# Kernel optimization log

Hardware: AMD Instinct MI355X
Metric: run time of the kernel (lower is better)

## Reference

```python
import math
import jax, jax.numpy as jnp
import numpy as np

B, T, D, H, HD, FF = 2, 2048, 768, 12, 64, 3072


def setup_inputs() -> dict:
    key = jax.random.key(0)
    ks = jax.random.split(key, 9)
    s = 0.02  # init scale
    x = jax.random.normal(ks[0], (B, T, D), jnp.float32)
    wq = jax.random.normal(ks[1], (D, D), jnp.float32) * s
    wk = jax.random.normal(ks[2], (D, D), jnp.float32) * s
    wv = jax.random.normal(ks[3], (D, D), jnp.float32) * s
    wo = jax.random.normal(ks[4], (D, D), jnp.float32) * s
    w1 = jax.random.normal(ks[5], (FF, D), jnp.float32) * s
    w2 = jax.random.normal(ks[6], (FF, D), jnp.float32) * s
    w3 = jax.random.normal(ks[7], (D, FF), jnp.float32) * s
    attn_norm_w = jnp.ones((D,), jnp.float32)
    ffn_norm_w = jnp.ones((D,), jnp.float32)
    # interleaved RoPE cache: values pair-repeated along head_dim
    inv_freq = 1.0 / (10000.0 ** (np.arange(0, HD, 2, dtype=np.float32) / HD))
    freqs = np.arange(T, dtype=np.float32)[:, None] * inv_freq[None, :]  # [T, HD/2]
    emb = np.repeat(freqs, 2, axis=-1)  # [T, HD]
    cos = jnp.asarray(np.cos(emb), jnp.float32)[None, None]  # [1,1,T,HD]
    sin = jnp.asarray(np.sin(emb), jnp.float32)[None, None]
    return {"x": x, "wq": wq, "wk": wk, "wv": wv, "wo": wo,
            "w1": w1, "w2": w2, "w3": w3,
            "attn_norm_w": attn_norm_w, "ffn_norm_w": ffn_norm_w,
            "cos": cos, "sin": sin}


def _rmsnorm(x, w, eps=1e-6):
    n = jnp.linalg.norm(x, axis=-1, keepdims=True)
    return w * x / (n / math.sqrt(x.shape[-1]) + eps)


def _rotate_half(x):
    x1, x2 = x[..., ::2], x[..., 1::2]
    return jnp.stack((-x2, x1), axis=-1).reshape(x.shape)


def _attention(x, wq, wk, wv, wo, cos, sin):
    b, t, c = x.shape
    q = (x @ wq.T).reshape(b, t, H, HD).transpose(0, 2, 1, 3)  # [B,H,T,hd]
    k = (x @ wk.T).reshape(b, t, H, HD).transpose(0, 2, 1, 3)
    v = (x @ wv.T).reshape(b, t, H, HD).transpose(0, 2, 1, 3)
    c_, s_ = cos[:, :, :t, :], sin[:, :, :t, :]
    q = q * c_ + _rotate_half(q) * s_
    k = k * c_ + _rotate_half(k) * s_
    att = jnp.einsum('bhqd,bhkd->bhqk', q, k) / math.sqrt(HD)
    mask = jnp.triu(jnp.full((t, t), -jnp.inf, att.dtype), k=1)
    att = jax.nn.softmax(att + mask, axis=-1)
    y = jnp.einsum('bhqk,bhkd->bhqd', att, v)
    y = y.transpose(0, 2, 1, 3).reshape(b, t, c)
    return y @ wo.T


def reference(x, wq, wk, wv, wo, w1, w2, w3, attn_norm_w, ffn_norm_w, cos, sin):
    x = x + _attention(_rmsnorm(x, attn_norm_w), wq, wk, wv, wo, cos, sin)
    h = _rmsnorm(x, ffn_norm_w)
    ff = (jax.nn.silu(h @ w1.T) * (h @ w2.T)) @ w3.T
    return x + ff
```

## Files before the change

kernel.cpp:

```cpp
#include <hip/hip_runtime.h>
#include <hip/hip_bf16.h>
#include <math.h>

typedef __bf16 bf16;
typedef __bf16 bf16x4 __attribute__((ext_vector_type(4)));
typedef __bf16 bf16x8 __attribute__((ext_vector_type(8)));
typedef float floatx4 __attribute__((ext_vector_type(4)));

#define T_ 2048
#define D_ 768
#define H_ 12
#define HD_ 64
#define FF_ 3072
#define LOG2E 1.44269504f
#define LDP 72

__device__ __forceinline__ floatx4 mfma_bf16(bf16x8 a, bf16x8 b, floatx4 c) {
  return __builtin_amdgcn_mfma_f32_16x16x32_bf16(a, b, c, 0, 0, 0);
}

__device__ __forceinline__ void rms_row(const float* __restrict__ x,
                                        const float* __restrict__ wt,
                                        bf16* __restrict__ o, int row, int tid) {
  const long off = (long)row * D_;
  float vals[3];
  float ss = 0.f;
#pragma unroll
  for (int i = 0; i < 3; i++) {
    vals[i] = x[off + tid + i * 256];
    ss += vals[i] * vals[i];
  }
#pragma unroll
  for (int d = 1; d < 64; d <<= 1) ss += __shfl_xor(ss, d);
  __shared__ float wsum[4];
  if ((tid & 63) == 0) wsum[tid >> 6] = ss;
  __syncthreads();
  const float tot = wsum[0] + wsum[1] + wsum[2] + wsum[3];
  const float inv = 1.0f / (sqrtf(tot * (1.0f / 768.0f)) + 1e-6f);
#pragma unroll
  for (int i = 0; i < 3; i++)
    o[off + tid + i * 256] = (bf16)(vals[i] * inv * wt[tid + i * 256]);
}

__global__ __launch_bounds__(256)
void prep_k(const float* __restrict__ wq, const float* __restrict__ wk,
            const float* __restrict__ wv, const float* __restrict__ wo,
            const float* __restrict__ w1, const float* __restrict__ w2,
            const float* __restrict__ w3, bf16* __restrict__ o,
            const float* __restrict__ x, const float* __restrict__ anw,
            bf16* __restrict__ hn) {
  if (blockIdx.x >= 4608) {
    rms_row(x, anw, hn, blockIdx.x - 4608, threadIdx.x);
    return;
  }
  const long i = ((long)blockIdx.x * 256 + threadIdx.x) * 8;
  const float* s;
  if      (i <  589824) s = wq + i;
  else if (i < 1179648) s = wk + (i -  589824);
  else if (i < 1769472) s = wv + (i - 1179648);
  else if (i < 2359296) s = wo + (i - 1769472);
  else if (i < 4718592) s = w1 + (i - 2359296);
  else if (i < 7077888) s = w2 + (i - 4718592);
  else                  s = w3 + (i - 7077888);
  const floatx4 a = *(const floatx4*)s;
  const floatx4 b = *(const floatx4*)(s + 4);
  bf16x8 r;
#pragma unroll
  for (int j = 0; j < 4; j++) { r[j] = (bf16)a[j]; r[4 + j] = (bf16)b[j]; }
  *(bf16x8*)&o[i] = r;
}

__global__ __launch_bounds__(256)
void rmsnorm_k(const float* __restrict__ x, const float* __restrict__ wt,
               bf16* __restrict__ o) {
  rms_row(x, wt, o, blockIdx.x, threadIdx.x);
}

__global__ __launch_bounds__(256)
void gemm_qkv(const bf16* __restrict__ A, const bf16* __restrict__ wq,
              const bf16* __restrict__ wk, const bf16* __restrict__ wv,
              bf16* __restrict__ q, bf16* __restrict__ k, bf16* __restrict__ vt,
              const float* __restrict__ cosb, const float* __restrict__ sinb) {
  const int widx = blockIdx.x / 6;
  const int nb   = blockIdx.x % 6;
  const bf16* W = (widx == 0) ? wq : (widx == 1) ? wk : wv;
  const int m0 = blockIdx.y * 128, n0 = nb * 128;
  const int K = D_;

  __shared__ __align__(16) bf16 As[128 * LDP];
  __shared__ __align__(16) bf16 Ws[128 * LDP];

  const int tid = threadIdx.x;
  const int lane = tid & 63;
  const int wm = tid >> 7;
  const int wn = (tid >> 6) & 1;
  const int fr = lane & 15;
  const int fk = (lane >> 4) * 8;

  floatx4 acc[4][4] = {};

  const int ar = tid >> 3;
  const int ac = (tid & 7) * 8;
  const bf16* Aptr = A + (long)(m0 + ar) * K + ac;
  const bf16* Wptr = W + (long)(n0 + ar) * K + ac;
  const long rstep = (long)32 * K;

  bf16x8 apf[4], wpf[4];
#pragma unroll
  for (int c = 0; c < 4; c++) apf[c] = *(const bf16x8*)(Aptr + c * rstep);
#pragma unroll
  for (int c = 0; c < 4; c++) wpf[c] = *(const bf16x8*)(Wptr + c * rstep);

  const int ns = K >> 6;
  for (int ks = 0; ks < ns; ks++) {
    __syncthreads();
#pragma unroll
    for (int c = 0; c < 4; c++) *(bf16x8*)&As[(ar + c * 32) * LDP + ac] = apf[c];
#pragma unroll
    for (int c = 0; c < 4; c++) *(bf16x8*)&Ws[(ar + c * 32) * LDP + ac] = wpf[c];
    __syncthreads();
    const long koff = (long)((ks + 1 < ns) ? ks + 1 : ks) * 64;
#pragma unroll
    for (int c = 0; c < 4; c++) apf[c] = *(const bf16x8*)(Aptr + koff + c * rstep);
#pragma unroll
    for (int c = 0; c < 4; c++) wpf[c] = *(const bf16x8*)(Wptr + koff + c * rstep);
#pragma unroll
    for (int kc = 0; kc < 2; kc++) {
      bf16x8 af[4], bfv[4];
#pragma unroll
      for (int i = 0; i < 4; i++) af[i]  = *(const bf16x8*)&As[(wm * 64 + i * 16 + fr) * LDP + kc * 32 + fk];
#pragma unroll
      for (int j = 0; j < 4; j++) bfv[j] = *(const bf16x8*)&Ws[(wn * 64 + j * 16 + fr) * LDP + kc * 32 + fk];
#pragma unroll
      for (int i = 0; i < 4; i++)
#pragma unroll
        for (int j = 0; j < 4; j++)
          acc[i][j] = mfma_bf16(af[i], bfv[j], acc[i][j]);
    }
  }

  const int rb = (lane >> 4) * 4;
  if (widx < 2) {
    bf16* O = (widx == 0) ? q : k;
    const float sgn = (fr & 1) ? 1.f : -1.f;
#pragma unroll
    for (int i = 0; i < 4; i++)
#pragma unroll
      for (int j = 0; j < 4; j++) {
        const int n = n0 + wn * 64 + j * 16 + fr;
        const int d = n & 63;
#pragma unroll
        for (int r = 0; r < 4; r++) {
          const int m = m0 + wm * 64 + i * 16 + rb + r;
          const int pos = m & (T_ - 1);
          const float val = acc[i][j][r];
          const float par = __shfl_xor(val, 1);
          const float cc = cosb[pos * HD_ + d];
          const float ss = sinb[pos * HD_ + d];
          O[(long)m * D_ + n] = (bf16)(val * cc + sgn * par * ss);
        }
      }
  } else {
#pragma unroll
    for (int i = 0; i < 4; i++)
#pragma unroll
      for (int j = 0; j < 4; j++) {
        const int n = n0 + wn * 64 + j * 16 + fr;
        const int m = m0 + wm * 64 + i * 16 + rb;
        const int b = m >> 11;
        const int t = m & (T_ - 1);
        const long row = (long)(b * H_ + (n >> 6)) * HD_ + (n & 63);
        bf16x4 pk;
#pragma unroll
        for (int r = 0; r < 4; r++) pk[r] = (bf16)acc[i][j][r];
        *(bf16x4*)&vt[row * T_ + t] = pk;
      }
  }
}

__global__ __launch_bounds__(256)
void gemm_n64(const bf16* __restrict__ A, const bf16* __restrict__ W,
              float* __restrict__ C, const float* __restrict__ resid,
              int N, int K) {
  __shared__ __align__(16) bf16 As[128 * LDP];
  __shared__ __align__(16) bf16 Ws[64 * LDP];

  const int L  = blockIdx.x;
  const int j  = L >> 3;
  const int mb = (L & 7) * 4 + (j / 12);
  const int nb = j % 12;
  const int m0 = mb * 128, n0 = nb * 64;

  const int tid = threadIdx.x;
  const int lane = tid & 63;
  const int wm = tid >> 7;
  const int wn = (tid >> 6) & 1;
  const int fr = lane & 15;
  const int fk = (lane >> 4) * 8;

  floatx4 acc[4][2] = {};

  const int ar = tid >> 3;
  const int ac = (tid & 7) * 8;
  const bf16* Aptr = A + (long)(m0 + ar) * K + ac;
  const bf16* Wptr = W + (long)(n0 + ar) * K + ac;
  const long rstep = (long)32 * K;

  bf16x8 apf[4], wpf[2];
#pragma unroll
  for (int c = 0; c < 4; c++) apf[c] = *(const bf16x8*)(Aptr + c * rstep);
#pragma unroll
  for (int c = 0; c < 2; c++) wpf[c] = *(const bf16x8*)(Wptr + c * rstep);

  const int ns = K >> 6;
  for (int ks = 0; ks < ns; ks++) {
    __syncthreads();
#pragma unroll
    for (int c = 0; c < 4; c++) *(bf16x8*)&As[(ar + c * 32) * LDP + ac] = apf[c];
#pragma unroll
    for (int c = 0; c < 2; c++) *(bf16x8*)&Ws[(ar + c * 32) * LDP + ac] = wpf[c];
    __syncthreads();
    const long koff = (long)((ks + 1 < ns) ? ks + 1 : ks) * 64;
#pragma unroll
    for (int c = 0; c < 4; c++) apf[c] = *(const bf16x8*)(Aptr + koff + c * rstep);
#pragma unroll
    for (int c = 0; c < 2; c++) wpf[c] = *(const bf16x8*)(Wptr + koff + c * rstep);
#pragma unroll
    for (int kc = 0; kc < 2; kc++) {
      bf16x8 af[4], bfv[2];
#pragma unroll
      for (int i = 0; i < 4; i++) af[i]  = *(const bf16x8*)&As[(wm * 64 + i * 16 + fr) * LDP + kc * 32 + fk];
#pragma unroll
      for (int j2 = 0; j2 < 2; j2++) bfv[j2] = *(const bf16x8*)&Ws[(wn * 32 + j2 * 16 + fr) * LDP + kc * 32 + fk];
#pragma unroll
      for (int i = 0; i < 4; i++)
#pragma unroll
        for (int j2 = 0; j2 < 2; j2++)
          acc[i][j2] = mfma_bf16(af[i], bfv[j2], acc[i][j2]);
    }
  }

  const int rb = (lane >> 4) * 4;
#pragma unroll
  for (int i = 0; i < 4; i++)
#pragma unroll
    for (int j2 = 0; j2 < 2; j2++) {
      const int n = n0 + wn * 32 + j2 * 16 + fr;
#pragma unroll
      for (int r = 0; r < 4; r++) {
        const int m = m0 + wm * 64 + i * 16 + rb + r;
        const long idx = (long)m * N + n;
        C[idx] = acc[i][j2][r] + resid[idx];
      }
    }
}

__global__ __launch_bounds__(256)
void gemm_w3sk(const bf16* __restrict__ A, const bf16* __restrict__ W,
               float* __restrict__ p0, float* __restrict__ p1) {
  __shared__ __align__(16) bf16 As[128 * LDP];
  __shared__ __align__(16) bf16 Ws[64 * LDP];

  const int L  = blockIdx.x;
  const int j  = L >> 3;
  const int mb = (L & 7) * 4 + (j / 24);
  const int inner = j % 24;
  const int s  = inner / 12;
  const int nb = inner % 12;
  const int m0 = mb * 128, n0 = nb * 64;
  const int K = FF_;
  const int kbase = s * 1536;
  float* C = s ? p1 : p0;

  const int tid = threadIdx.x;
  const int lane = tid & 63;
  const int wm = tid >> 7;
  const int wn = (tid >> 6) & 1;
  const int fr = lane & 15;
  const int fk = (lane >> 4) * 8;

  floatx4 acc[4][2] = {};

  const int ar = tid >> 3;
  const int ac = (tid & 7) * 8;
  const bf16* Aptr = A + (long)(m0 + ar) * K + kbase + ac;
  const bf16* Wptr = W + (long)(n0 + ar) * K + kbase + ac;
  const long rstep = (long)32 * K;

  bf16x8 apf[4], wpf[2];
#pragma unroll
  for (int c = 0; c < 4; c++) apf[c] = *(const bf16x8*)(Aptr + c * rstep);
#pragma unroll
  for (int c = 0; c < 2; c++) wpf[c] = *(const bf16x8*)(Wptr + c * rstep);

  const int ns = 24;
  for (int ks = 0; ks < ns; ks++) {
    __syncthreads();
#pragma unroll
    for (int c = 0; c < 4; c++) *(bf16x8*)&As[(ar + c * 32) * LDP + ac] = apf[c];
#pragma unroll
    for (int c = 0; c < 2; c++) *(bf16x8*)&Ws[(ar + c * 32) * LDP + ac] = wpf[c];
    __syncthreads();
    const long koff = (long)((ks + 1 < ns) ? ks + 1 : ks) * 64;
#pragma unroll
    for (int c = 0; c < 4; c++) apf[c] = *(const bf16x8*)(Aptr + koff + c * rstep);
#pragma unroll
    for (int c = 0; c < 2; c++) wpf[c] = *(const bf16x8*)(Wptr + koff + c * rstep);
#pragma unroll
    for (int kc = 0; kc < 2; kc++) {
      bf16x8 af[4], bfv[2];
#pragma unroll
      for (int i = 0; i < 4; i++) af[i]  = *(const bf16x8*)&As[(wm * 64 + i * 16 + fr) * LDP + kc * 32 + fk];
#pragma unroll
      for (int j2 = 0; j2 < 2; j2++) bfv[j2] = *(const bf16x8*)&Ws[(wn * 32 + j2 * 16 + fr) * LDP + kc * 32 + fk];
#pragma unroll
      for (int i = 0; i < 4; i++)
#pragma unroll
        for (int j2 = 0; j2 < 2; j2++)
          acc[i][j2] = mfma_bf16(af[i], bfv[j2], acc[i][j2]);
    }
  }

  const int rb = (lane >> 4) * 4;
#pragma unroll
  for (int i = 0; i < 4; i++)
#pragma unroll
    for (int j2 = 0; j2 < 2; j2++) {
      const int n = n0 + wn * 32 + j2 * 16 + fr;
#pragma unroll
      for (int r = 0; r < 4; r++) {
        const int m = m0 + wm * 64 + i * 16 + rb + r;
        C[(long)m * D_ + n] = acc[i][j2][r];
      }
    }
}

__global__ __launch_bounds__(256)
void comb3_k(const float* __restrict__ p0, const float* __restrict__ p1,
             const float* __restrict__ xm, float* __restrict__ out) {
  const long i = ((long)blockIdx.x * 256 + threadIdx.x) * 8;
#pragma unroll
  for (int c = 0; c < 2; c++) {
    const floatx4 a = *(const floatx4*)&p0[i + c * 4];
    const floatx4 b = *(const floatx4*)&p1[i + c * 4];
    const floatx4 d = *(const floatx4*)&xm[i + c * 4];
    floatx4 r;
#pragma unroll
    for (int e = 0; e < 4; e++) r[e] = a[e] + b[e] + d[e];
    *(floatx4*)&out[i + c * 4] = r;
  }
}

__global__ __launch_bounds__(256, 2)
void gemm_w12(const bf16* __restrict__ A, const bf16* __restrict__ W1,
              const bf16* __restrict__ W2, bf16* __restrict__ G) {
  __shared__ __align__(16) bf16 As[128 * LDP];
  __shared__ __align__(16) bf16 W1s[128 * LDP];
  __shared__ __align__(16) bf16 W2s[128 * LDP];

  const int L  = blockIdx.x;
  const int j  = L >> 3;
  const int mb = j / 3;
  const int nb = (L & 7) * 3 + (j % 3);
  const int m0 = mb * 128, n0 = nb * 128;
  const int K = D_;

  const int tid = threadIdx.x;
  const int lane = tid & 63;
  const int wm = tid >> 7;
  const int wn = (tid >> 6) & 1;
  const int fr = lane & 15;
  const int fk = (lane >> 4) * 8;

  floatx4 acc1[4][4] = {}, acc2[4][4] = {};

  const int ar = tid >> 3;
  const int ac = (tid & 7) * 8;
  const bf16* Aptr  = A  + (long)(m0 + ar) * K + ac;
  const bf16* W1ptr = W1 + (long)(n0 + ar) * K + ac;
  const bf16* W2ptr = W2 + (long)(n0 + ar) * K + ac;
  const long rstep = (long)32 * K;

  bf16x8 apf[4], w1pf[4], w2pf[4];
#pragma unroll
  for (int c = 0; c < 4; c++) { apf[c]  = *(const bf16x8*)(Aptr  + c * rstep);
                                w1pf[c] = *(const bf16x8*)(W1ptr + c * rstep);
                                w2pf[c] = *(const bf16x8*)(W2ptr + c * rstep); }

  const int ns = K >> 6;
  for (int ks = 0; ks < ns; ks++) {
    __syncthreads();
#pragma unroll
    for (int c = 0; c < 4; c++) { *(bf16x8*)&As[(ar + c * 32) * LDP + ac]  = apf[c];
                                  *(bf16x8*)&W1s[(ar + c * 32) * LDP + ac] = w1pf[c];
                                  *(bf16x8*)&W2s[(ar + c * 32) * LDP + ac] = w2pf[c]; }
    __syncthreads();
    const long koff = (long)((ks + 1 < ns) ? ks + 1 : ks) * 64;
#pragma unroll
    for (int c = 0; c < 4; c++) { apf[c]  = *(const bf16x8*)(Aptr  + koff + c * rstep);
                                  w1pf[c] = *(const bf16x8*)(W1ptr + koff + c * rstep);
                                  w2pf[c] = *(const bf16x8*)(W2ptr + koff + c * rstep); }
#pragma unroll
    for (int kc = 0; kc < 2; kc++) {
      bf16x8 af[4];
#pragma unroll
      for (int i = 0; i < 4; i++) af[i] = *(const bf16x8*)&As[(wm * 64 + i * 16 + fr) * LDP + kc * 32 + fk];
      {
        bf16x8 b1[4];
#pragma unroll
        for (int jj = 0; jj < 4; jj++) b1[jj] = *(const bf16x8*)&W1s[(wn * 64 + jj * 16 + fr) * LDP + kc * 32 + fk];
#pragma unroll
        for (int i = 0; i < 4; i++)
#pragma unroll
          for (int jj = 0; jj < 4; jj++)
            acc1[i][jj] = mfma_bf16(af[i], b1[jj], acc1[i][jj]);
      }
      {
        bf16x8 b2[4];
#pragma unroll
        for (int jj = 0; jj < 4; jj++) b2[jj] = *(const bf16x8*)&W2s[(wn * 64 + jj * 16 + fr) * LDP + kc * 32 + fk];
#pragma unroll
        for (int i = 0; i < 4; i++)
#pragma unroll
          for (int jj = 0; jj < 4; jj++)
            acc2[i][jj] = mfma_bf16(af[i], b2[jj], acc2[i][jj]);
      }
    }
  }

  const int rb = (lane >> 4) * 4;
#pragma unroll
  for (int i = 0; i < 4; i++)
#pragma unroll
    for (int jj = 0; jj < 4; jj++) {
      const int n = n0 + wn * 64 + jj * 16 + fr;
#pragma unroll
      for (int r = 0; r < 4; r++) {
        const int m = m0 + wm * 64 + i * 16 + rb + r;
        const float a1 = acc1[i][jj][r];
        const float a2 = acc2[i][jj][r];
        const float s = a1 / (1.f + exp2f(-a1 * LOG2E));
        G[(long)m * FF_ + n] = (bf16)(s * a2);
      }
    }
}

__global__ __launch_bounds__(256, 4)
void flash_attn(const bf16* __restrict__ q, const bf16* __restrict__ k,
                const bf16* __restrict__ vtg, float* __restrict__ po,
                float* __restrict__ pm, float* __restrict__ pl) {
  const int gid = blockIdx.x;
  const int bh = gid / 80;
  const int r  = gid % 80;
  int qt, c;
  if (r < 8)       { qt = r; c = 0; }
  else if (r < 24) { qt = 8 + ((r - 8) >> 1); c = (r - 8) & 1; }
  else if (r < 48) { const int u = r - 24; const int d = u / 3; qt = 16 + d; c = u - d * 3; }
  else             { const int u = r - 48; qt = 24 + (u >> 2); c = u & 3; }
  const int b  = bh / H_;
  const int h  = bh % H_;
  const int q0 = qt * 64;
  const int tbeg = c * 8;
  const int tend = (tbeg + 7 < qt) ? tbeg + 7 : qt;

  __shared__ __align__(16) bf16 Qs[64][72];
  __shared__ __align__(16) bf16 Ks[64][72];
  __shared__ __align__(16) bf16 Vt[64][72];
  __shared__ __align__(16) bf16 Ps[4][16][72];

  const int tid = threadIdx.x, lane = tid & 63, w = tid >> 6;
  const int fr = lane & 15, quad = lane >> 4, fk = quad * 8;
  const long base = ((long)b * T_) * D_ + h * HD_;
  const long vbase = (long)bh * HD_ * T_;

  {
    const int srow = tid >> 2, scol = (tid & 3) * 16;
    const long g = base + (long)(q0 + srow) * D_ + scol;
    *(bf16x8*)&Qs[srow][scol]     = *(const bf16x8*)&q[g];
    *(bf16x8*)&Qs[srow][scol + 8] = *(const bf16x8*)&q[g + 8];
  }

  float m_st = -1e30f, l_st = 0.f;
  floatx4 o[4] = {};
  const float SC = 0.125f * LOG2E;

  for (int t = tbeg; t <= tend; t++) {
    const int k0 = t * 64;
    __syncthreads();
    {
      const int srow = tid >> 2, scol = (tid & 3) * 16;
      const long kg = base + (long)(k0 + srow) * D_ + scol;
      *(bf16x8*)&Ks[srow][scol]     = *(const bf16x8*)&k[kg];
      *(bf16x8*)&Ks[srow][scol + 8] = *(const bf16x8*)&k[kg + 8];
      const long vg = vbase + (long)srow * T_ + k0 + scol;
      *(bf16x8*)&Vt[srow][scol]     = *(const bf16x8*)&vtg[vg];
      *(bf16x8*)&Vt[srow][scol + 8] = *(const bf16x8*)&vtg[vg + 8];
    }
    __syncthreads();

    floatx4 s[4] = {};
#pragma unroll
    for (int kd = 0; kd < 2; kd++) {
      const bf16x8 bq = *(const bf16x8*)&Qs[w * 16 + fr][kd * 32 + fk];
#pragma unroll
      for (int kt = 0; kt < 4; kt++) {
        const bf16x8 ak = *(const bf16x8*)&Ks[kt * 16 + fr][kd * 32 + fk];
        s[kt] = mfma_bf16(ak, bq, s[kt]);
      }
    }

    if (t == qt) {
      const int qloc = w * 16 + fr;
#pragma unroll
      for (int kt = 0; kt < 4; kt++)
#pragma unroll
        for (int r2 = 0; r2 < 4; r2++) {
          const int kvloc = kt * 16 + quad * 4 + r2;
          s[kt][r2] = (kvloc > qloc) ? -1e30f : s[kt][r2] * SC;
        }
    } else {
#pragma unroll
      for (int kt = 0; kt < 4; kt++)
#pragma unroll
        for (int r2 = 0; r2 < 4; r2++) s[kt][r2] *= SC;
    }

    float mx = -1e30f;
#pragma unroll
    for (int kt = 0; kt < 4; kt++)
#pragma unroll
      for (int r2 = 0; r2 < 4; r2++) mx = fmaxf(mx, s[kt][r2]);
    mx = fmaxf(mx, __shfl_xor(mx, 16));
    mx = fmaxf(mx, __shfl_xor(mx, 32));
    const float mnew  = fmaxf(m_st, mx);
    const float alpha = exp2f(m_st - mnew);
    m_st = mnew;
    float rs = 0.f;
#pragma unroll
    for (int kt = 0; kt < 4; kt++)
#pragma unroll
      for (int r2 = 0; r2 < 4; r2++) {
        const float pv = exp2f(s[kt][r2] - mnew);
        s[kt][r2] = pv;
        rs += pv;
      }
    rs += __shfl_xor(rs, 16);
    rs += __shfl_xor(rs, 32);
    l_st = l_st * alpha + rs;
#pragma unroll
    for (int ht = 0; ht < 4; ht++) o[ht] *= alpha;

#pragma unroll
    for (int kt = 0; kt < 4; kt++) {
      bf16x4 pk;
#pragma unroll
      for (int r2 = 0; r2 < 4; r2++) pk[r2] = (bf16)s[kt][r2];
      *(bf16x4*)&Ps[w][fr][kt * 16 + quad * 4] = pk;
    }

#pragma unroll
    for (int kq = 0; kq < 2; kq++) {
      const bf16x8 bp = *(const bf16x8*)&Ps[w][fr][kq * 32 + fk];
#pragma unroll
      for (int ht = 0; ht < 4; ht++) {
        const bf16x8 av = *(const bf16x8*)&Vt[ht * 16 + fr][kq * 32 + fk];
        o[ht] = mfma_bf16(av, bp, o[ht]);
      }
    }
  }

  const int qq = w * 16 + fr;
  const long pg = (long)gid * 4096 + qq * 64;
#pragma unroll
  for (int ht = 0; ht < 4; ht++)
    *(floatx4*)&po[pg + ht * 16 + quad * 4] = o[ht];
  if (quad == 0) { pm[gid * 64 + qq] = m_st; pl[gid * 64 + qq] = l_st; }
}

__global__ __launch_bounds__(256)
void flash_comb(const float* __restrict__ po, const float* __restrict__ pm,
                const float* __restrict__ pl, bf16* __restrict__ y) {
  const int bh = blockIdx.x >> 5;
  const int qt = blockIdx.x & 31;
  const int b = bh / H_, h = bh % H_;
  const int nc = (qt >> 3) + 1;
  int bse;
  if      (qt <  8) bse = qt;
  else if (qt < 16) bse = 8  + 2 * (qt - 8);
  else if (qt < 24) bse = 24 + 3 * (qt - 16);
  else              bse = 48 + 4 * (qt - 24);
  const int g0 = bh * 80 + bse;

  const int t = threadIdx.x;
  const int qq = t >> 2, hg = (t & 3) * 16;

  float M = -1e30f;
  for (int c2 = 0; c2 < nc; c2++) M = fmaxf(M, pm[(g0 + c2) * 64 + qq]);
  float l = 0.f;
  floatx4 o[4] = {};
  for (int c2 = 0; c2 < nc; c2++) {
    const float wgt = exp2f(pm[(g0 + c2) * 64 + qq] - M);
    l += wgt * pl[(g0 + c2) * 64 + qq];
    const long pg = (long)(g0 + c2) * 4096 + qq * 64 + hg;
#pragma unroll
    for (int j = 0; j < 4; j++) {
      const floatx4 t4 = *(const floatx4*)&po[pg + j * 4];
#pragma unroll
      for (int e = 0; e < 4; e++) o[j][e] += wgt * t4[e];
    }
  }
  const float inv = 1.f / l;
  bf16x8 r0, r1;
#pragma unroll
  for (int e = 0; e < 4; e++) {
    r0[e]     = (bf16)(o[0][e] * inv);
    r0[4 + e] = (bf16)(o[1][e] * inv);
    r1[e]     = (bf16)(o[2][e] * inv);
    r1[4 + e] = (bf16)(o[3][e] * inv);
  }
  const long yoff = ((long)b * T_ + qt * 64 + qq) * D_ + h * HD_ + hg;
  *(bf16x8*)&y[yoff]     = r0;
  *(bf16x8*)&y[yoff + 8] = r1;
}

extern "C" void kernel_launch(void* const* d_in, const int* in_sizes, int n_in,
                              void* d_out, int out_size, void* d_ws, size_t ws_size,
                              hipStream_t stream) {
  const float* x    = (const float*)d_in[0];
  const float* wq   = (const float*)d_in[1];
  const float* wk   = (const float*)d_in[2];
  const float* wv   = (const float*)d_in[3];
  const float* wo   = (const float*)d_in[4];
  const float* w1   = (const float*)d_in[5];
  const float* w2   = (const float*)d_in[6];
  const float* w3   = (const float*)d_in[7];
  const float* anw  = (const float*)d_in[8];
  const float* fnw  = (const float*)d_in[9];
  const float* cosb = (const float*)d_in[10];
  const float* sinb = (const float*)d_in[11];

  char* ws = (char*)d_ws;
  bf16*  wb  = (bf16*)(ws + 0);
  bf16*  wqb = wb;
  bf16*  wkb = wb +  589824;
  bf16*  wvb = wb + 1179648;
  bf16*  wob = wb + 1769472;
  bf16*  w1b = wb + 2359296;
  bf16*  w2b = wb + 4718592;
  bf16*  w3b = wb + 7077888;
  bf16*  qb  = (bf16*)(ws + 18874368);
  bf16*  kb  = (bf16*)(ws + 25165824);
  bf16*  vt  = (bf16*)(ws + 31457280);
  bf16*  yb  = (bf16*)(ws + 37748736);
  bf16*  hn  = (bf16*)(ws + 44040192);
  float* xm  = (float*)(ws + 50331648);
  bf16*  g   = (bf16*)(ws + 62914560);
  float* po  = (float*)(ws + 50331648);
  float* pm  = (float*)(ws + 81788928);
  float* pl  = (float*)(ws + 82280448);
  float* p30 = (float*)(ws + 18874368);
  float* p31 = (float*)(ws + 37748736);

  prep_k<<<8704, 256, 0, stream>>>(wq, wk, wv, wo, w1, w2, w3, wb, x, anw, hn);
  gemm_qkv<<<dim3(18, 32), 256, 0, stream>>>(hn, wqb, wkb, wvb, qb, kb, vt, cosb, sinb);
  flash_attn<<<1920, 256, 0, stream>>>(qb, kb, vt, po, pm, pl);
  flash_comb<<<768, 256, 0, stream>>>(po, pm, pl, yb);
  gemm_n64<<<384, 256, 0, stream>>>(yb, wob, xm, x, 768, 768);
  rmsnorm_k<<<4096, 256, 0, stream>>>(xm, fnw, hn);
  gemm_w12<<<768, 256, 0, stream>>>(hn, w1b, w2b, g);
  gemm_w3sk<<<768, 256, 0, stream>>>(g, w3b, p30, p31);
  comb3_k<<<1536, 256, 0, stream>>>(p30, p31, xm, (float*)d_out);
}
```

Baseline: 298.5 us.

## Prefetch next K/V tile into registers and interleave head blocks in flash attention

The flash attention kernel now loads the next key/value tile into registers while the current tile is being computed, then writes it to shared memory at the start of the next iteration. This hides global memory latency behind the MFMA work. The block index mapping also changes to batch-head fastest (gid%24), so blocks with similar causal work run close together and load stays balanced. The combine kernel's partial-result indexing is updated to match. The prefetch adds register pressure under a 4-blocks-per-SM launch bound.

```diff
diff --git a/kernel.cpp b/kernel.cpp
--- a/kernel.cpp
+++ b/kernel.cpp
@@ -450,8 +450,8 @@
                 const bf16* __restrict__ vtg, float* __restrict__ po,
                 float* __restrict__ pm, float* __restrict__ pl) {
   const int gid = blockIdx.x;
-  const int bh = gid / 80;
-  const int r  = gid % 80;
+  const int bh = gid % 24;
+  const int r  = gid / 24;
   int qt, c;
   if (r < 8)       { qt = r; c = 0; }
   else if (r < 24) { qt = 8 + ((r - 8) >> 1); c = (r - 8) & 1; }
@@ -473,30 +473,36 @@
   const long base = ((long)b * T_) * D_ + h * HD_;
   const long vbase = (long)bh * HD_ * T_;
 
+  const int srow = tid >> 2, scol = (tid & 3) * 16;
   {
-    const int srow = tid >> 2, scol = (tid & 3) * 16;
     const long g = base + (long)(q0 + srow) * D_ + scol;
     *(bf16x8*)&Qs[srow][scol]     = *(const bf16x8*)&q[g];
     *(bf16x8*)&Qs[srow][scol + 8] = *(const bf16x8*)&q[g + 8];
   }
 
+  const bf16* kgp = k + base + (long)srow * D_ + scol;
+  const bf16* vgp = vtg + vbase + (long)srow * T_ + scol;
+  bf16x8 kpf0 = *(const bf16x8*)(kgp + (long)tbeg * 64 * D_);
+  bf16x8 kpf1 = *(const bf16x8*)(kgp + (long)tbeg * 64 * D_ + 8);
+  bf16x8 vpf0 = *(const bf16x8*)(vgp + tbeg * 64);
+  bf16x8 vpf1 = *(const bf16x8*)(vgp + tbeg * 64 + 8);
+
   float m_st = -1e30f, l_st = 0.f;
   floatx4 o[4] = {};
   const float SC = 0.125f * LOG2E;
 
   for (int t = tbeg; t <= tend; t++) {
-    const int k0 = t * 64;
-    __syncthreads();
-    {
-      const int srow = tid >> 2, scol = (tid & 3) * 16;
-      const long kg = base + (long)(k0 + srow) * D_ + scol;
-      *(bf16x8*)&Ks[srow][scol]     = *(const bf16x8*)&k[kg];
-      *(bf16x8*)&Ks[srow][scol + 8] = *(const bf16x8*)&k[kg + 8];
-      const long vg = vbase + (long)srow * T_ + k0 + scol;
-      *(bf16x8*)&Vt[srow][scol]     = *(const bf16x8*)&vtg[vg];
-      *(bf16x8*)&Vt[srow][scol + 8] = *(const bf16x8*)&vtg[vg + 8];
-    }
-    __syncthreads();
+    __syncthreads();
+    *(bf16x8*)&Ks[srow][scol]     = kpf0;
+    *(bf16x8*)&Ks[srow][scol + 8] = kpf1;
+    *(bf16x8*)&Vt[srow][scol]     = vpf0;
+    *(bf16x8*)&Vt[srow][scol + 8] = vpf1;
+    __syncthreads();
+    const int tn = (t + 1 <= tend) ? t + 1 : t;
+    kpf0 = *(const bf16x8*)(kgp + (long)tn * 64 * D_);
+    kpf1 = *(const bf16x8*)(kgp + (long)tn * 64 * D_ + 8);
+    vpf0 = *(const bf16x8*)(vgp + tn * 64);
+    vpf1 = *(const bf16x8*)(vgp + tn * 64 + 8);
 
     floatx4 s[4] = {};
 #pragma unroll
@@ -589,19 +595,19 @@
   else if (qt < 16) bse = 8  + 2 * (qt - 8);
   else if (qt < 24) bse = 24 + 3 * (qt - 16);
   else              bse = 48 + 4 * (qt - 24);
-  const int g0 = bh * 80 + bse;
 
   const int t = threadIdx.x;
   const int qq = t >> 2, hg = (t & 3) * 16;
 
   float M = -1e30f;
-  for (int c2 = 0; c2 < nc; c2++) M = fmaxf(M, pm[(g0 + c2) * 64 + qq]);
+  for (int c2 = 0; c2 < nc; c2++) M = fmaxf(M, pm[((bse + c2) * 24 + bh) * 64 + qq]);
   float l = 0.f;
   floatx4 o[4] = {};
   for (int c2 = 0; c2 < nc; c2++) {
-    const float wgt = exp2f(pm[(g0 + c2) * 64 + qq] - M);
-    l += wgt * pl[(g0 + c2) * 64 + qq];
-    const long pg = (long)(g0 + c2) * 4096 + qq * 64 + hg;
+    const int g = (bse + c2) * 24 + bh;
+    const float wgt = exp2f(pm[g * 64 + qq] - M);
+    l += wgt * pl[g * 64 + qq];
+    const long pg = (long)g * 4096 + qq * 64 + hg;
 #pragma unroll
     for (int j = 0; j < 4; j++) {
       const floatx4 t4 = *(const floatx4*)&po[pg + j * 4];
```

Measured after the change: 293.1 us (median of 2 runs). No clear change (-1.8%).
